# Optimization experiments

Measured on AMD Instinct MI355X. Metric: run time of the kernel, lower is better.

The kernel has to match this reference:

```python
import jax, jax.numpy as jnp
import numpy as np

N_OUT = 4096
N_IN = 4096
TOKENS = 8192
BITWIDTH = 4
GROUP_SIZE = 128
ZERO = 2 ** (BITWIDTH - 1)  # symmetric GPTQ zero-point


def setup_inputs() -> dict:
    key = jax.random.key(0)
    kx, kq, ks = jax.random.split(key, 3)
    x = jax.random.normal(kx, (TOKENS, N_IN), dtype=jnp.float32)
    qweight = jax.random.randint(kq, (N_OUT, N_IN), 0, 2 ** BITWIDTH, dtype=jnp.int32)
    scales = jax.random.uniform(ks, (N_OUT, N_IN // GROUP_SIZE), dtype=jnp.float32) * 0.02 + 0.001
    return {"x": x, "qweight": qweight, "scales": scales}


def reference(x, qweight, scales):
    # Dequantize: W[o, i] = (q[o, i] - zero) * scales[o, i // group_size]
    q = qweight.astype(x.dtype) - jnp.asarray(ZERO, dtype=x.dtype)
    # reshape input dim into (n_groups, group_size) and broadcast group scales
    qg = q.reshape(N_OUT, N_IN // GROUP_SIZE, GROUP_SIZE)
    w = (qg * scales[:, :, None].astype(x.dtype)).reshape(N_OUT, N_IN)
    # out = x @ W^T  -> [tokens, n_out]
    return jnp.einsum('ti,oi->to', x, w)
```

## Files before the change

kernel.cpp:

```cpp
#include <hip/hip_runtime.h>
#include <hip/hip_bf16.h>
#include <stdint.h>

#define TOKENS_C 8192
#define NIN_C    4096
#define NOUT_C   4096
#define GROUP_C  128
#define QZERO_C  8

typedef __bf16 bf16_t;
typedef __bf16  bf16x8 __attribute__((ext_vector_type(8)));
typedef float   f32x4  __attribute__((ext_vector_type(4)));
typedef int     i32x4  __attribute__((ext_vector_type(4)));

#define GAS __attribute__((address_space(1)))
#define LAS __attribute__((address_space(3)))

__device__ __forceinline__ void gload16(const void* g, void* l) {
  __builtin_amdgcn_global_load_lds((const GAS void*)g, (LAS void*)l, 16, 0, 0);
}

__global__ __launch_bounds__(256) void dequant_w_kernel(
    const int* __restrict__ qw, const float* __restrict__ sc,
    bf16_t* __restrict__ wb)
{
  const int t = blockIdx.x * 256 + threadIdx.x;
  const int64_t base = (int64_t)t * 8;
  const int o = (int)(base >> 12);
  const int i = (int)(base & 4095);
  const float s = sc[(o << 5) | (i >> 7)];
  i32x4 q0 = *(const i32x4*)(qw + base);
  i32x4 q1 = *(const i32x4*)(qw + base + 4);
  bf16x8 r;
  r[0] = (bf16_t)((float)(q0[0] - QZERO_C) * s);
  r[1] = (bf16_t)((float)(q0[1] - QZERO_C) * s);
  r[2] = (bf16_t)((float)(q0[2] - QZERO_C) * s);
  r[3] = (bf16_t)((float)(q0[3] - QZERO_C) * s);
  r[4] = (bf16_t)((float)(q1[0] - QZERO_C) * s);
  r[5] = (bf16_t)((float)(q1[1] - QZERO_C) * s);
  r[6] = (bf16_t)((float)(q1[2] - QZERO_C) * s);
  r[7] = (bf16_t)((float)(q1[3] - QZERO_C) * s);
  *(bf16x8*)(wb + base) = r;
}

__global__ __launch_bounds__(256) void cvt_x_kernel(
    const float* __restrict__ x, bf16_t* __restrict__ xb)
{
  const int t = blockIdx.x * 256 + threadIdx.x;
  const int64_t base = (int64_t)t * 8;
  f32x4 a = *(const f32x4*)(x + base);
  f32x4 b = *(const f32x4*)(x + base + 4);
  bf16x8 r;
  r[0] = (bf16_t)a[0]; r[1] = (bf16_t)a[1]; r[2] = (bf16_t)a[2]; r[3] = (bf16_t)a[3];
  r[4] = (bf16_t)b[0]; r[5] = (bf16_t)b[1]; r[6] = (bf16_t)b[2]; r[7] = (bf16_t)b[3];
  *(bf16x8*)(xb + base) = r;
}

#define BM 256
#define BN 256
#define BK 64
#define NT (NIN_C / BK)

__global__ __launch_bounds__(512, 2) void gemm_bt_kernel(
    const bf16_t* __restrict__ A,
    const bf16_t* __restrict__ B,
    float* __restrict__ C)
{
  constexpr int K = NIN_C, N = NOUT_C;
  __shared__ char smem[131072];

  const int tid  = threadIdx.x;
  const int lane = tid & 63;
  const int wid  = tid >> 6;
  const int wm   = wid >> 2;
  const int wn   = wid & 3;
  const int bm   = blockIdx.x;
  const int bn   = blockIdx.y;

  const int l8   = lane >> 3;
  const int c8   = lane & 7;
  const int cswz = ((c8 ^ l8) << 4);
  const char* Ab = (const char*)A;
  const char* Bb = (const char*)B;
  int64_t aBase[4], bBase[4];
#pragma unroll
  for (int l = 0; l < 4; ++l) {
    const int slot = (wid << 2) + l;
    aBase[l] = ((int64_t)(bm * BM + slot * 8 + l8) * K) * 2 + cswz;
    bBase[l] = ((int64_t)(bn * BN + slot * 8 + l8) * K) * 2 + cswz;
  }
  const int ldst = ((wid << 2) << 10) + (lane << 4);

  const int frow  = lane & 15;
  const int fcolb = (lane >> 4) << 4;
  const int rsw   = (lane & 7) << 4;

  f32x4 acc[8][4] = {};

  {
    char* Ad = smem;
    char* Bd = smem + 65536;
#pragma unroll
    for (int l = 0; l < 4; ++l) gload16(Ab + aBase[l], Ad + ldst + (l << 10));
#pragma unroll
    for (int l = 0; l < 4; ++l) gload16(Bb + bBase[l], Bd + ldst + (l << 10));
  }
  asm volatile("s_waitcnt vmcnt(0)" ::: "memory");
  __builtin_amdgcn_s_barrier();
  __builtin_amdgcn_sched_barrier(0);

  int cur = 0;
  for (int t = 0; t < NT; ++t) {
    const char* Ar = smem + cur * 32768;
    const char* Br = smem + 65536 + cur * 32768;
    char* Aw = smem + (cur ^ 1) * 32768;
    char* Bw = smem + 65536 + (cur ^ 1) * 32768;
    const int64_t koff = (int64_t)(t + 1) * (BK * 2);
    const bool pf = (t + 1 < NT);

    bf16x8 a[4], b[4];
#pragma unroll
    for (int p = 0; p < 4; ++p) {
      const int mh = p & 1;
      const int kk = p >> 1;

      if (p == 0 && pf) {
#pragma unroll
        for (int l = 0; l < 4; ++l) gload16(Ab + aBase[l] + koff, Aw + ldst + (l << 10));
      }
      if (p == 1 && pf) {
#pragma unroll
        for (int l = 0; l < 4; ++l) gload16(Bb + bBase[l] + koff, Bw + ldst + (l << 10));
      }

      const int cb = (kk << 6) + fcolb;
      if (mh == 0) {
#pragma unroll
        for (int j = 0; j < 4; ++j) {
          const int row = wn * 64 + j * 16 + frow;
          b[j] = *(const bf16x8*)(Br + row * 128 + (cb ^ rsw));
        }
      }
#pragma unroll
      for (int i = 0; i < 4; ++i) {
        const int row = wm * 128 + (mh * 4 + i) * 16 + frow;
        a[i] = *(const bf16x8*)(Ar + row * 128 + (cb ^ rsw));
      }

      __builtin_amdgcn_s_setprio(1);
#pragma unroll
      for (int i = 0; i < 4; ++i)
#pragma unroll
        for (int j = 0; j < 4; ++j)
          acc[mh * 4 + i][j] =
              __builtin_amdgcn_mfma_f32_16x16x32_bf16(a[i], b[j], acc[mh * 4 + i][j], 0, 0, 0);
      __builtin_amdgcn_s_setprio(0);
      if (p < 3) __builtin_amdgcn_s_barrier();
    }

    asm volatile("s_waitcnt vmcnt(0)" ::: "memory");
    __builtin_amdgcn_s_barrier();
    __builtin_amdgcn_sched_barrier(0);
    cur ^= 1;
  }

  const int crow0 = bm * BM + wm * 128;
  const int ccol0 = bn * BN + wn * 64;
  const int r0 = (lane >> 4) << 2;
  const int cc = lane & 15;
#pragma unroll
  for (int fi = 0; fi < 8; ++fi)
#pragma unroll
    for (int j = 0; j < 4; ++j) {
      f32x4 v = acc[fi][j];
#pragma unroll
      for (int r = 0; r < 4; ++r)
        C[(int64_t)(crow0 + fi * 16 + r0 + r) * N + (ccol0 + j * 16 + cc)] = v[r];
    }
}

__global__ __launch_bounds__(256) void naive_kernel(
    const float* __restrict__ x, const int* __restrict__ qw,
    const float* __restrict__ sc, float* __restrict__ out)
{
  const int64_t idx = (int64_t)blockIdx.x * 256 + threadIdx.x;
  const int tok = (int)(idx >> 12);
  const int o   = (int)(idx & 4095);
  const float* xr = x + (int64_t)tok * NIN_C;
  const int* qr = qw + (int64_t)o * NIN_C;
  float acc = 0.f;
  for (int g = 0; g < NIN_C / GROUP_C; ++g) {
    float s = sc[(o << 5) | g];
    float ga = 0.f;
#pragma unroll 4
    for (int i = g * GROUP_C; i < (g + 1) * GROUP_C; ++i)
      ga += xr[i] * (float)(qr[i] - QZERO_C);
    acc += s * ga;
  }
  out[idx] = acc;
}

extern "C" void kernel_launch(void* const* d_in, const int* in_sizes, int n_in,
                              void* d_out, int out_size, void* d_ws, size_t ws_size,
                              hipStream_t stream) {
  const float* x  = (const float*)d_in[0];
  const int*   qw = (const int*)d_in[1];
  const float* sc = (const float*)d_in[2];
  float* out = (float*)d_out;

  const size_t xb_bytes = (size_t)TOKENS_C * NIN_C * sizeof(bf16_t);
  const size_t wb_bytes = (size_t)NOUT_C * NIN_C * sizeof(bf16_t);

  if (ws_size < xb_bytes + wb_bytes) {
    const int64_t total = (int64_t)TOKENS_C * NOUT_C;
    naive_kernel<<<(int)(total / 256), 256, 0, stream>>>(x, qw, sc, out);
    return;
  }

  bf16_t* xb = (bf16_t*)d_ws;
  bf16_t* wb = (bf16_t*)((char*)d_ws + xb_bytes);

  {
    const int64_t elems = (int64_t)TOKENS_C * NIN_C;
    cvt_x_kernel<<<(int)(elems / 8 / 256), 256, 0, stream>>>(x, xb);
  }
  {
    const int64_t elems = (int64_t)NOUT_C * NIN_C;
    dequant_w_kernel<<<(int)(elems / 8 / 256), 256, 0, stream>>>(qw, sc, wb);
  }
  {
    dim3 grid(TOKENS_C / BM, NOUT_C / BN);
    gemm_bt_kernel<<<grid, 512, 0, stream>>>(xb, wb, out);
  }
}
```

Measured before the change: 276.8 us.

## Switch GEMM to 4-stage LDS pipeline with BK=32 and partial vmcnt waits

Replaces the double-buffered BK=64 main loop with a four-slot ring of BK=32 tiles, keeping three tiles in flight and waiting with vmcnt(8) instead of draining all loads each iteration. The LDS layout and XOR swizzle are reworked for 64-byte rows, and a tail loop handles the last three tiles. The aim is to hide global-load latency behind MFMA work. The cost is twice as many iterations and barriers per K, plus a more fragile swizzle and wait accounting.

```diff
diff --git a/kernel.cpp b/kernel.cpp
--- a/kernel.cpp
+++ b/kernel.cpp
@@ -58,7 +58,7 @@
 
 #define BM 256
 #define BN 256
-#define BK 64
+#define BK 32
 #define NT (NIN_C / BK)
 
 __global__ __launch_bounds__(512, 2) void gemm_bt_kernel(
@@ -67,6 +67,7 @@
     float* __restrict__ C)
 {
   constexpr int K = NIN_C, N = NOUT_C;
+  constexpr int K2 = K * 2;
   __shared__ char smem[131072];
 
   const int tid  = threadIdx.x;
@@ -77,92 +78,101 @@
   const int bm   = blockIdx.x;
   const int bn   = blockIdx.y;
 
-  const int l8   = lane >> 3;
-  const int c8   = lane & 7;
-  const int cswz = ((c8 ^ l8) << 4);
+  const int srow0 = wid * 32 + (lane >> 2);
+  const int ssw   = ((lane >> 2) & 3) ^ ((lane >> 4) & 3);
+  const int scswz = (((lane & 3) ^ ssw) << 4);
   const char* Ab = (const char*)A;
   const char* Bb = (const char*)B;
-  int64_t aBase[4], bBase[4];
-#pragma unroll
-  for (int l = 0; l < 4; ++l) {
-    const int slot = (wid << 2) + l;
-    aBase[l] = ((int64_t)(bm * BM + slot * 8 + l8) * K) * 2 + cswz;
-    bBase[l] = ((int64_t)(bn * BN + slot * 8 + l8) * K) * 2 + cswz;
-  }
-  const int ldst = ((wid << 2) << 10) + (lane << 4);
-
-  const int frow  = lane & 15;
-  const int fcolb = (lane >> 4) << 4;
-  const int rsw   = (lane & 7) << 4;
+  const int64_t aoff0 = (int64_t)(bm * BM + srow0)      * K2 + scswz;
+  const int64_t aoff1 = (int64_t)(bm * BM + srow0 + 16) * K2 + scswz;
+  const int64_t boff0 = (int64_t)(bn * BN + srow0)      * K2 + scswz;
+  const int64_t boff1 = (int64_t)(bn * BN + srow0 + 16) * K2 + scswz;
+  const int sdst = wid * 2048 + (lane << 4);
+
+#define STAGE_A(tt) { char* d_ = smem + (((tt) & 3) << 14) + sdst;             \
+    gload16(Ab + aoff0 + (int64_t)(tt) * 64, d_);                              \
+    gload16(Ab + aoff1 + (int64_t)(tt) * 64, d_ + 1024); }
+#define STAGE_B(tt) { char* d_ = smem + 65536 + (((tt) & 3) << 14) + sdst;     \
+    gload16(Bb + boff0 + (int64_t)(tt) * 64, d_);                              \
+    gload16(Bb + boff1 + (int64_t)(tt) * 64, d_ + 1024); }
+
+  const int frow = lane & 15;
+  const int fcb  = (((lane >> 4) ^ (lane & 3) ^ ((lane >> 2) & 3)) & 3) << 4
+                 | (((lane >> 4) << 4) & ~0x30);
+  const int fcb2 = (((lane >> 4) ^ ((lane & 3) ^ ((lane >> 2) & 3))) << 4);
 
   f32x4 acc[8][4] = {};
 
-  {
-    char* Ad = smem;
-    char* Bd = smem + 65536;
-#pragma unroll
-    for (int l = 0; l < 4; ++l) gload16(Ab + aBase[l], Ad + ldst + (l << 10));
-#pragma unroll
-    for (int l = 0; l < 4; ++l) gload16(Bb + bBase[l], Bd + ldst + (l << 10));
-  }
+  STAGE_A(0); STAGE_B(0);
+  STAGE_A(1); STAGE_B(1);
+  STAGE_A(2); STAGE_B(2);
+  asm volatile("s_waitcnt vmcnt(8)" ::: "memory");
+  __builtin_amdgcn_s_barrier();
+  __builtin_amdgcn_sched_barrier(0);
+
+  for (int t = 0; t < NT - 3; ++t) {
+    const char* Ar = smem + ((t & 3) << 14);
+    const char* Br = smem + 65536 + ((t & 3) << 14);
+    bf16x8 a[4], b[4];
+
+#pragma unroll
+    for (int j = 0; j < 4; ++j)
+      b[j] = *(const bf16x8*)(Br + (wn * 64 + j * 16 + frow) * 64 + fcb2);
+#pragma unroll
+    for (int i = 0; i < 4; ++i)
+      a[i] = *(const bf16x8*)(Ar + (wm * 128 + i * 16 + frow) * 64 + fcb2);
+    STAGE_A(t + 3);
+    __builtin_amdgcn_s_barrier();
+    __builtin_amdgcn_s_setprio(1);
+#pragma unroll
+    for (int i = 0; i < 4; ++i)
+#pragma unroll
+      for (int j = 0; j < 4; ++j)
+        acc[i][j] = __builtin_amdgcn_mfma_f32_16x16x32_bf16(a[i], b[j], acc[i][j], 0, 0, 0);
+    __builtin_amdgcn_s_setprio(0);
+    __builtin_amdgcn_s_barrier();
+
+#pragma unroll
+    for (int i = 0; i < 4; ++i)
+      a[i] = *(const bf16x8*)(Ar + (wm * 128 + (4 + i) * 16 + frow) * 64 + fcb2);
+    STAGE_B(t + 3);
+    __builtin_amdgcn_s_barrier();
+    __builtin_amdgcn_s_setprio(1);
+#pragma unroll
+    for (int i = 0; i < 4; ++i)
+#pragma unroll
+      for (int j = 0; j < 4; ++j)
+        acc[4 + i][j] = __builtin_amdgcn_mfma_f32_16x16x32_bf16(a[i], b[j], acc[4 + i][j], 0, 0, 0);
+    __builtin_amdgcn_s_setprio(0);
+    asm volatile("s_waitcnt vmcnt(8)" ::: "memory");
+    __builtin_amdgcn_s_barrier();
+    __builtin_amdgcn_sched_barrier(0);
+  }
+
   asm volatile("s_waitcnt vmcnt(0)" ::: "memory");
   __builtin_amdgcn_s_barrier();
   __builtin_amdgcn_sched_barrier(0);
-
-  int cur = 0;
-  for (int t = 0; t < NT; ++t) {
-    const char* Ar = smem + cur * 32768;
-    const char* Br = smem + 65536 + cur * 32768;
-    char* Aw = smem + (cur ^ 1) * 32768;
-    char* Bw = smem + 65536 + (cur ^ 1) * 32768;
-    const int64_t koff = (int64_t)(t + 1) * (BK * 2);
-    const bool pf = (t + 1 < NT);
-
+  for (int t = NT - 3; t < NT; ++t) {
+    const char* Ar = smem + ((t & 3) << 14);
+    const char* Br = smem + 65536 + ((t & 3) << 14);
     bf16x8 a[4], b[4];
 #pragma unroll
-    for (int p = 0; p < 4; ++p) {
-      const int mh = p & 1;
-      const int kk = p >> 1;
-
-      if (p == 0 && pf) {
-#pragma unroll
-        for (int l = 0; l < 4; ++l) gload16(Ab + aBase[l] + koff, Aw + ldst + (l << 10));
-      }
-      if (p == 1 && pf) {
-#pragma unroll
-        for (int l = 0; l < 4; ++l) gload16(Bb + bBase[l] + koff, Bw + ldst + (l << 10));
-      }
-
-      const int cb = (kk << 6) + fcolb;
-      if (mh == 0) {
-#pragma unroll
-        for (int j = 0; j < 4; ++j) {
-          const int row = wn * 64 + j * 16 + frow;
-          b[j] = *(const bf16x8*)(Br + row * 128 + (cb ^ rsw));
-        }
-      }
-#pragma unroll
-      for (int i = 0; i < 4; ++i) {
-        const int row = wm * 128 + (mh * 4 + i) * 16 + frow;
-        a[i] = *(const bf16x8*)(Ar + row * 128 + (cb ^ rsw));
-      }
-
-      __builtin_amdgcn_s_setprio(1);
+    for (int j = 0; j < 4; ++j)
+      b[j] = *(const bf16x8*)(Br + (wn * 64 + j * 16 + frow) * 64 + fcb2);
+#pragma unroll
+    for (int mh = 0; mh < 2; ++mh) {
+#pragma unroll
+      for (int i = 0; i < 4; ++i)
+        a[i] = *(const bf16x8*)(Ar + (wm * 128 + (mh * 4 + i) * 16 + frow) * 64 + fcb2);
 #pragma unroll
       for (int i = 0; i < 4; ++i)
 #pragma unroll
         for (int j = 0; j < 4; ++j)
           acc[mh * 4 + i][j] =
               __builtin_amdgcn_mfma_f32_16x16x32_bf16(a[i], b[j], acc[mh * 4 + i][j], 0, 0, 0);
-      __builtin_amdgcn_s_setprio(0);
-      if (p < 3) __builtin_amdgcn_s_barrier();
     }
-
-    asm volatile("s_waitcnt vmcnt(0)" ::: "memory");
-    __builtin_amdgcn_s_barrier();
-    __builtin_amdgcn_sched_barrier(0);
-    cur ^= 1;
-  }
+  }
+  (void)fcb;
 
   const int crow0 = bm * BM + wm * 128;
   const int ccol0 = bn * BN + wn * 64;
@@ -177,6 +187,8 @@
       for (int r = 0; r < 4; ++r)
         C[(int64_t)(crow0 + fi * 16 + r0 + r) * N + (ccol0 + j * 16 + cc)] = v[r];
     }
+#undef STAGE_A
+#undef STAGE_B
 }
 
 __global__ __launch_bounds__(256) void naive_kernel(
```

New measurement: 300.1 us. +8.4%, slower.
